# Optimization experiments

Measured on AMD Instinct MI355X. Metric: run time of the kernel, lower is better.

Reference implementation:

```python
import jax, jax.numpy as jnp
import numpy as np

B, N, I = 8, 1024, 64
E, H, D = 2, 2, 128   # edge types, heads per layer, hidden dim
O = 64                # num_outputs
IN1 = E * H * D       # layer-1 filter input dim (concat of layer-0 heads)


def setup_inputs() -> dict:
    key = jax.random.key(0)
    ks = jax.random.split(key, 20)
    s = lambda f: 1.0 / np.sqrt(f)
    inp = {
        "nodes": jax.random.normal(ks[0], (B, N, I), jnp.float32),
        "edges": jax.random.normal(ks[1], (B, N, N, E), jnp.float32) * 0.1,
        "Wemb": jax.random.normal(ks[2], (I, D), jnp.float32) * s(I),
        "bemb": jnp.zeros((D,), jnp.float32),
        # layer 0 params: filter W, att nets a1/a2 (weight + bias), state bias
        "W0":   jax.random.normal(ks[3], (E, H, D, D), jnp.float32) * s(D),
        "A1w0": jax.random.normal(ks[4], (E, H, D), jnp.float32) * s(D),
        "A1b0": jnp.zeros((E, H), jnp.float32),
        "A2w0": jax.random.normal(ks[5], (E, H, D), jnp.float32) * s(D),
        "A2b0": jnp.zeros((E, H), jnp.float32),
        "SB0":  jnp.zeros((E, H, D), jnp.float32),
        # layer 1 params (input dim = E*H*D from concat)
        "W1":   jax.random.normal(ks[6], (E, H, IN1, D), jnp.float32) * s(IN1),
        "A1w1": jax.random.normal(ks[7], (E, H, D), jnp.float32) * s(D),
        "A1b1": jnp.zeros((E, H), jnp.float32),
        "A2w1": jax.random.normal(ks[8], (E, H, D), jnp.float32) * s(D),
        "A2b1": jnp.zeros((E, H), jnp.float32),
        "SB1":  jnp.zeros((E, H, D), jnp.float32),
        "Wout": jax.random.normal(ks[9], (D, O), jnp.float32) * s(D),
        "bout": jnp.zeros((O,), jnp.float32),
    }
    return inp


def _gat_layer(state, edges_ebnn, W, a1w, a1b, a2w, a2b, sb):
    # state: (B,N,Fin); W: (E,H,Fin,D); edges_ebnn: (E,1,B,N,N)
    Wh = jnp.einsum('bni,ehid->ehbnd', state, W)                    # (E,H,B,N,D)
    s1 = jnp.einsum('ehbnd,ehd->ehbn', Wh, a1w) + a1b[:, :, None, None]
    s2 = jnp.einsum('ehbnd,ehd->ehbn', Wh, a2w) + a2b[:, :, None, None]
    att = s1[..., :, None] + s2[..., None, :]                       # a1_i + a2_j
    att = jax.nn.leaky_relu(att, 0.2) + edges_ebnn                  # edge-type bias
    att = jax.nn.softmax(att, axis=-2)                              # torch dim=1 (over i)
    msg = jnp.einsum('ehbij,ehbjd->ehbid', att, Wh)                 # bmm aggregation
    return msg + sb[:, :, None, None, :]                            # (E,H,B,N,D)


def reference(nodes, edges, Wemb, bemb,
              W0, A1w0, A1b0, A2w0, A2b0, SB0,
              W1, A1w1, A1b1, A2w1, A2b1, SB1,
              Wout, bout):
    edges_e = jnp.transpose(edges, (3, 0, 1, 2))[:, None]           # (E,1,B,N,N)
    state = jax.nn.relu(nodes @ Wemb + bemb)                        # SlimFC embedding
    # layer 0: concat heads/edgetypes along feature dim (torch order jj outer, ii inner)
    m0 = _gat_layer(state, edges_e, W0, A1w0, A1b0, A2w0, A2b0, SB0)
    state = jnp.transpose(m0, (2, 3, 0, 1, 4)).reshape(B, N, E * H * D)
    # layer 1 (last): elu then mean over all heads/edgetypes
    m1 = jax.nn.elu(_gat_layer(state, edges_e, W1, A1w1, A1b1, A2w1, A2b1, SB1))
    state = jnp.mean(m1, axis=(0, 1))                               # (B,N,D)
    return state @ Wout + bout                                      # (B,N,O)
```

## Files before the change

### kernel.cpp

```cpp
#include <hip/hip_runtime.h>
#include <hip/hip_bf16.h>
#include <math.h>

#define NB 8
#define NN 1024
#define NI 64
#define EHC 4
#define ND 128
#define NO 64
#define FIN1 512
#define BN 8192

typedef __attribute__((ext_vector_type(8))) short short8;
typedef __attribute__((ext_vector_type(4))) float f32x4;

__device__ __forceinline__ unsigned short f2bf(float f) {
    union { float f; unsigned u; } v; v.f = f;
    unsigned r = v.u + 0x7FFF + ((v.u >> 16) & 1);
    return (unsigned short)(r >> 16);
}

__global__ void prepTk(const float* __restrict__ W0, const float* __restrict__ W1,
                       const float* __restrict__ Wemb, unsigned short* __restrict__ W0T,
                       unsigned short* __restrict__ W1T, unsigned short* __restrict__ WembT) {
    int idx = blockIdx.x * 256 + threadIdx.x;
    if (idx < EHC * ND * ND) {
        int eh = idx >> 14, d = (idx >> 7) & 127, k = idx & 127;
        W0T[idx] = f2bf(W0[((size_t)(eh * ND + k)) * ND + d]);
    }
    int idx1 = idx - EHC * ND * ND;
    if (idx1 >= 0 && idx1 < EHC * ND * FIN1) {
        int eh = idx1 >> 16;
        int r = idx1 & 65535;
        int d = r >> 9, k = r & 511;
        W1T[idx1] = f2bf(W1[((size_t)(eh * FIN1 + k)) * ND + d]);
    }
    int idx2 = idx - (EHC * ND * ND + EHC * ND * FIN1);
    if (idx2 >= 0 && idx2 < ND * NI) {
        int d = idx2 >> 6, k = idx2 & 63;
        WembT[idx2] = f2bf(Wemb[k * ND + d]);
    }
}

__global__ __launch_bounds__(256, 4) void embwh0k(
    const float* __restrict__ nodes, const unsigned short* __restrict__ WembT,
    const float* __restrict__ bemb, const unsigned short* __restrict__ W0T,
    unsigned short* __restrict__ WhT, const float* __restrict__ a1w,
    const float* __restrict__ a1b, const float* __restrict__ a2w,
    const float* __restrict__ a2b, float* __restrict__ s1, float* __restrict__ s2) {
    int id = blockIdx.x;
    int g = id & 7, s_ = id >> 3;
    int eh = s_ & 3;
    int row0 = ((s_ >> 2) * 8 + g) * 32;
    int t = threadIdx.x;
    int w = t >> 6, lane = t & 63;
    int m = lane & 15, quad = lane >> 4;

    __shared__ unsigned short stateL[32 * 136];

    f32x4 accE[2][2];
#pragma unroll
    for (int mt = 0; mt < 2; ++mt)
#pragma unroll
        for (int nt = 0; nt < 2; ++nt) accE[mt][nt] = (f32x4){0.f, 0.f, 0.f, 0.f};
#pragma unroll
    for (int kt = 0; kt < 2; ++kt) {
        short8 aE[2], bE[2];
#pragma unroll
        for (int mt = 0; mt < 2; ++mt) {
            const float* np = nodes + (size_t)(row0 + mt * 16 + m) * NI + kt * 32 + quad * 8;
            f32x4 v0 = *(const f32x4*)np;
            f32x4 v1 = *(const f32x4*)(np + 4);
            union { unsigned short us[8]; short8 s8; } pk;
#pragma unroll
            for (int r = 0; r < 4; ++r) {
                pk.us[r] = f2bf(v0[r]);
                pk.us[r + 4] = f2bf(v1[r]);
            }
            aE[mt] = pk.s8;
        }
#pragma unroll
        for (int nt = 0; nt < 2; ++nt)
            bE[nt] = *(const short8*)(WembT + (w * 32 + nt * 16 + m) * NI + kt * 32 + quad * 8);
#pragma unroll
        for (int mt = 0; mt < 2; ++mt)
#pragma unroll
            for (int nt = 0; nt < 2; ++nt)
                accE[mt][nt] =
                    __builtin_amdgcn_mfma_f32_16x16x32_bf16(aE[mt], bE[nt], accE[mt][nt], 0, 0, 0);
    }
#pragma unroll
    for (int mt = 0; mt < 2; ++mt)
#pragma unroll
        for (int nt = 0; nt < 2; ++nt) {
            int d = w * 32 + nt * 16 + m;
            float bb = bemb[d];
#pragma unroll
            for (int r = 0; r < 4; ++r) {
                float v = fmaxf(accE[mt][nt][r] + bb, 0.f);
                stateL[(mt * 16 + quad * 4 + r) * 136 + d] = f2bf(v);
            }
        }
    __syncthreads();

    f32x4 acc[2][2];
#pragma unroll
    for (int mt = 0; mt < 2; ++mt)
#pragma unroll
        for (int nt = 0; nt < 2; ++nt) acc[mt][nt] = (f32x4){0.f, 0.f, 0.f, 0.f};
#pragma unroll
    for (int k0 = 0; k0 < ND; k0 += 32) {
        short8 a[2], b[2];
#pragma unroll
        for (int mt = 0; mt < 2; ++mt)
            a[mt] = *(const short8*)&stateL[(mt * 16 + m) * 136 + k0 + quad * 8];
#pragma unroll
        for (int nt = 0; nt < 2; ++nt)
            b[nt] = *(const short8*)(W0T + ((size_t)(eh * ND + w * 32 + nt * 16 + m)) * ND +
                                     k0 + quad * 8);
#pragma unroll
        for (int mt = 0; mt < 2; ++mt)
#pragma unroll
            for (int nt = 0; nt < 2; ++nt)
                acc[mt][nt] =
                    __builtin_amdgcn_mfma_f32_16x16x32_bf16(a[mt], b[nt], acc[mt][nt], 0, 0, 0);
    }

    int b_ = row0 >> 10, i0b = row0 & 1023;
    int ehb = eh * NB + b_;
#pragma unroll
    for (int mt = 0; mt < 2; ++mt)
#pragma unroll
        for (int nt = 0; nt < 2; ++nt) {
            int d = w * 32 + nt * 16 + m;
            int i = i0b + mt * 16 + quad * 4;
            union { unsigned short us[4]; unsigned long long u64; } pk;
#pragma unroll
            for (int r = 0; r < 4; ++r) pk.us[r] = f2bf(acc[mt][nt][r]);
            *(unsigned long long*)(WhT + (((size_t)ehb) * ND + d) * NN + i) = pk.u64;
        }
    float w1a = a1w[eh * ND + w * 32 + m], w1b = a1w[eh * ND + w * 32 + 16 + m];
    float w2a = a2w[eh * ND + w * 32 + m], w2b = a2w[eh * ND + w * 32 + 16 + m];
    float p1[2][4], p2[2][4];
#pragma unroll
    for (int mt = 0; mt < 2; ++mt)
#pragma unroll
        for (int r = 0; r < 4; ++r) {
            p1[mt][r] = acc[mt][0][r] * w1a + acc[mt][1][r] * w1b;
            p2[mt][r] = acc[mt][0][r] * w2a + acc[mt][1][r] * w2b;
        }
#pragma unroll
    for (int off = 8; off >= 1; off >>= 1)
#pragma unroll
        for (int mt = 0; mt < 2; ++mt)
#pragma unroll
            for (int r = 0; r < 4; ++r) {
                p1[mt][r] += __shfl_xor(p1[mt][r], off);
                p2[mt][r] += __shfl_xor(p2[mt][r], off);
            }
    __shared__ float sred[2][4][4][8];
    if (m == 0) {
#pragma unroll
        for (int mt = 0; mt < 2; ++mt)
#pragma unroll
            for (int r = 0; r < 4; ++r) {
                sred[0][w][quad][mt * 4 + r] = p1[mt][r];
                sred[1][w][quad][mt * 4 + r] = p2[mt][r];
            }
    }
    __syncthreads();
    if (t < 32) {
        int mt = t >> 4, quad2 = (t >> 2) & 3, r = t & 3;
        int c = mt * 4 + r;
        float v = sred[0][0][quad2][c] + sred[0][1][quad2][c] + sred[0][2][quad2][c] +
                  sred[0][3][quad2][c];
        s1[(size_t)ehb * NN + i0b + t] = v + a1b[eh];
    } else if (t < 64) {
        int tl = t - 32;
        int mt = tl >> 4, quad2 = (tl >> 2) & 3, r = tl & 3;
        int c = mt * 4 + r;
        float v = sred[1][0][quad2][c] + sred[1][1][quad2][c] + sred[1][2][quad2][c] +
                  sred[1][3][quad2][c];
        s2[(size_t)ehb * NN + i0b + tl] = v + a2b[eh];
    }
}

__global__ __launch_bounds__(256, 4) void whgemm1k(
    const unsigned short* __restrict__ state, const unsigned short* __restrict__ WT,
    unsigned short* __restrict__ WhT, const float* __restrict__ a1w,
    const float* __restrict__ a1b, const float* __restrict__ a2w,
    const float* __restrict__ a2b, float* __restrict__ s1, float* __restrict__ s2) {
    int id = blockIdx.x;
    int g = id & 7, s_ = id >> 3;
    int eh = s_ & 3;
    int row0 = ((s_ >> 2) * 8 + g) * 32;
    int t = threadIdx.x;
    int w = t >> 6, lane = t & 63;
    int m = lane & 15, quad = lane >> 4;

    f32x4 acc[2][2];
#pragma unroll
    for (int mt = 0; mt < 2; ++mt)
#pragma unroll
        for (int nt = 0; nt < 2; ++nt) acc[mt][nt] = (f32x4){0.f, 0.f, 0.f, 0.f};

    const unsigned short* Ab = state + (size_t)(row0 + m) * FIN1 + quad * 8;
    const unsigned short* Bb = WT + ((size_t)eh * ND + w * 32 + m) * FIN1 + quad * 8;
#pragma unroll 4
    for (int k0 = 0; k0 < FIN1; k0 += 32) {
        short8 a[2], b[2];
#pragma unroll
        for (int mt = 0; mt < 2; ++mt)
            a[mt] = *(const short8*)(Ab + (size_t)mt * 16 * FIN1 + k0);
#pragma unroll
        for (int nt = 0; nt < 2; ++nt)
            b[nt] = *(const short8*)(Bb + (size_t)nt * 16 * FIN1 + k0);
#pragma unroll
        for (int mt = 0; mt < 2; ++mt)
#pragma unroll
            for (int nt = 0; nt < 2; ++nt)
                acc[mt][nt] =
                    __builtin_amdgcn_mfma_f32_16x16x32_bf16(a[mt], b[nt], acc[mt][nt], 0, 0, 0);
    }
    int b_ = row0 >> 10, i0b = row0 & 1023;
    int ehb = eh * NB + b_;
#pragma unroll
    for (int mt = 0; mt < 2; ++mt)
#pragma unroll
        for (int nt = 0; nt < 2; ++nt) {
            int d = w * 32 + nt * 16 + m;
            int i = i0b + mt * 16 + quad * 4;
            union { unsigned short us[4]; unsigned long long u64; } pk;
#pragma unroll
            for (int r = 0; r < 4; ++r) pk.us[r] = f2bf(acc[mt][nt][r]);
            *(unsigned long long*)(WhT + (((size_t)ehb) * ND + d) * NN + i) = pk.u64;
        }
    float w1a = a1w[eh * ND + w * 32 + m], w1b = a1w[eh * ND + w * 32 + 16 + m];
    float w2a = a2w[eh * ND + w * 32 + m], w2b = a2w[eh * ND + w * 32 + 16 + m];
    float p1[2][4], p2[2][4];
#pragma unroll
    for (int mt = 0; mt < 2; ++mt)
#pragma unroll
        for (int r = 0; r < 4; ++r) {
            p1[mt][r] = acc[mt][0][r] * w1a + acc[mt][1][r] * w1b;
            p2[mt][r] = acc[mt][0][r] * w2a + acc[mt][1][r] * w2b;
        }
#pragma unroll
    for (int off = 8; off >= 1; off >>= 1)
#pragma unroll
        for (int mt = 0; mt < 2; ++mt)
#pragma unroll
            for (int r = 0; r < 4; ++r) {
                p1[mt][r] += __shfl_xor(p1[mt][r], off);
                p2[mt][r] += __shfl_xor(p2[mt][r], off);
            }
    __shared__ float sred[2][4][4][8];
    if (m == 0) {
#pragma unroll
        for (int mt = 0; mt < 2; ++mt)
#pragma unroll
            for (int r = 0; r < 4; ++r) {
                sred[0][w][quad][mt * 4 + r] = p1[mt][r];
                sred[1][w][quad][mt * 4 + r] = p2[mt][r];
            }
    }
    __syncthreads();
    if (t < 32) {
        int mt = t >> 4, quad2 = (t >> 2) & 3, r = t & 3;
        int c = mt * 4 + r;
        float v = sred[0][0][quad2][c] + sred[0][1][quad2][c] + sred[0][2][quad2][c] +
                  sred[0][3][quad2][c];
        s1[(size_t)ehb * NN + i0b + t] = v + a1b[eh];
    } else if (t < 64) {
        int tl = t - 32;
        int mt = tl >> 4, quad2 = (tl >> 2) & 3, r = tl & 3;
        int c = mt * 4 + r;
        float v = sred[1][0][quad2][c] + sred[1][1][quad2][c] + sred[1][2][quad2][c] +
                  sred[1][3][quad2][c];
        s2[(size_t)ehb * NN + i0b + tl] = v + a2b[eh];
    }
}

__global__ __launch_bounds__(256, 4) void colsumk(const float* __restrict__ edges,
                                                  const float* __restrict__ s1,
                                                  const float* __restrict__ s2,
                                                  float* __restrict__ Spart) {
    int jt = blockIdx.x, b = blockIdx.y, ic = blockIdx.z;
    int t = threadIdx.x;
    int jp = t & 31, is = t >> 5;
    int j = jt * 64 + jp * 2;
    __shared__ float s1L[4][128];
    for (int idx = t; idx < 512; idx += 256) {
        int eh = idx >> 7;
        s1L[eh][idx & 127] = s1[((size_t)eh * NB + b) * NN + ic * 128 + (idx & 127)];
    }
    __syncthreads();
    float s2v[4][2], acc4[4][2];
#pragma unroll
    for (int eh = 0; eh < 4; ++eh) {
        s2v[eh][0] = s2[((size_t)eh * NB + b) * NN + j];
        s2v[eh][1] = s2[((size_t)eh * NB + b) * NN + j + 1];
        acc4[eh][0] = 0.f;
        acc4[eh][1] = 0.f;
    }
    const float4* ep = (const float4*)edges +
                       (size_t)(b * NN + ic * 128 + is * 16) * (NN / 2) + jt * 32 + jp;
#pragma unroll 4
    for (int ii = 0; ii < 16; ++ii) {
        float4 ev = ep[(size_t)ii * (NN / 2)];
        float s1v = s1L[0][is * 16 + ii];
#pragma unroll
        for (int eh = 0; eh < 4; ++eh) {
            float sv = s1L[eh][is * 16 + ii];
            float x0 = sv + s2v[eh][0];
            x0 = fmaxf(x0, 0.2f * x0);
            acc4[eh][0] += __expf(x0 + (eh < 2 ? ev.x : ev.y));
            float x1 = sv + s2v[eh][1];
            x1 = fmaxf(x1, 0.2f * x1);
            acc4[eh][1] += __expf(x1 + (eh < 2 ? ev.z : ev.w));
        }
        (void)s1v;
    }
    __shared__ float red[8][4][64];
#pragma unroll
    for (int eh = 0; eh < 4; ++eh) {
        red[is][eh][jp * 2] = acc4[eh][0];
        red[is][eh][jp * 2 + 1] = acc4[eh][1];
    }
    __syncthreads();
    if (t < 256) {
        int eho = t >> 6, jlo = t & 63;
        float Sv = 0.f;
#pragma unroll
        for (int isx = 0; isx < 8; ++isx) Sv += red[isx][eho][jlo];
        Spart[(((size_t)ic * EHC + eho) * NB + b) * NN + jt * 64 + jlo] = Sv;
    }
}

__global__ __launch_bounds__(512, 4) void msgk(const float* __restrict__ edges,
                                               const unsigned short* __restrict__ WhT,
                                               const float* __restrict__ s1,
                                               const float* __restrict__ s2,
                                               const float* __restrict__ Spart,
                                               const float* __restrict__ sb,
                                               unsigned short* __restrict__ out0,
                                               float* __restrict__ out1, int mode) {
    int id = blockIdx.x;
    int b = id & 7;
    int s_ = id >> 3;
    int eh = s_ & 3;
    int itile = s_ >> 2;
    int e = eh >> 1;
    int i0 = itile * 64;
    int t = threadIdx.x;
    int w = t >> 6, lane = t & 63;
    int n = lane & 15, quad = lane >> 4;
    int jl = t & 63, ib = w;

    __shared__ float2 stL[NN];
    __shared__ unsigned short pA[2][64 * 72];

    int base = (eh * NB + b) * NN;
    const size_t pstr = (size_t)EHC * NB * NN;
    for (int jj = t; jj < NN; jj += 512) {
        float S = 0.f;
#pragma unroll
        for (int ic = 0; ic < 8; ++ic) S += Spart[(size_t)ic * pstr + base + jj];
        stL[jj] = make_float2(s2[base + jj], __logf(S));
    }
    float s1r[8];
    {
        const f32x4* sp = (const f32x4*)(s1 + base + i0 + ib * 8);
        f32x4 v0 = sp[0], v1 = sp[1];
#pragma unroll
        for (int r = 0; r < 4; ++r) { s1r[r] = v0[r]; s1r[r + 4] = v1[r]; }
    }

    f32x4 acc[4];
#pragma unroll
    for (int nt = 0; nt < 4; ++nt) acc[nt] = (f32x4){0.f, 0.f, 0.f, 0.f};

    const unsigned short* Ab =
        WhT + ((size_t)base * ND + (size_t)(w * 16 + n) * NN) + quad * 8;
    const float2* ep = (const float2*)edges + (size_t)(b * NN + i0 + ib * 8) * NN + jl;
    __syncthreads();

    float2 evA[8], evB[8];
    short8 aA[2], aB[2];

    auto loadE = [&](float2* ev, int j0) {
#pragma unroll
        for (int q = 0; q < 8; ++q) ev[q] = ep[(size_t)q * NN + j0];
    };
    auto loadA = [&](short8* av, int j0) {
#pragma unroll
        for (int kt = 0; kt < 2; ++kt)
            av[kt] = *(const short8*)(Ab + kt * 32 + j0);
    };
    auto pstep = [&](const float2* ev, const short8* av, int j0, int buf) {
        float2 stj = stL[j0 + jl];
#pragma unroll
        for (int q = 0; q < 8; ++q) {
            float edge = e ? ev[q].y : ev[q].x;
            float x = s1r[q] + stj.x;
            x = fmaxf(x, 0.2f * x);
            pA[buf][(ib * 8 + q) * 72 + jl] = f2bf(__expf(x + edge - stj.y));
        }
        __syncthreads();
#pragma unroll
        for (int kt = 0; kt < 2; ++kt) {
            short8 bv[4];
#pragma unroll
            for (int nt = 0; nt < 4; ++nt)
                bv[nt] = *(const short8*)&pA[buf][(nt * 16 + n) * 72 + kt * 32 + quad * 8];
#pragma unroll
            for (int nt = 0; nt < 4; ++nt)
                acc[nt] =
                    __builtin_amdgcn_mfma_f32_16x16x32_bf16(av[kt], bv[nt], acc[nt], 0, 0, 0);
        }
    };

    loadE(evA, 0);
    loadA(aA, 0);
    for (int sp2 = 0; sp2 < 8; ++sp2) {
        int j0 = sp2 * 128;
        loadE(evB, j0 + 64);
        loadA(aB, j0 + 64);
        pstep(evA, aA, j0, 0);
        if (sp2 < 7) {
            loadE(evA, j0 + 128);
            loadA(aA, j0 + 128);
        }
        pstep(evB, aB, j0 + 64, 1);
    }

    {
        int d0 = w * 16 + quad * 4;
        f32x4 sbv = *(const f32x4*)&sb[eh * ND + d0];
#pragma unroll
        for (int nt = 0; nt < 4; ++nt) {
            int i = i0 + nt * 16 + n;
            if (mode == 0) {
                union { unsigned short us[4]; unsigned long long u64; } pk;
#pragma unroll
                for (int r = 0; r < 4; ++r) pk.us[r] = f2bf(acc[nt][r] + sbv[r]);
                *(unsigned long long*)(out0 + (size_t)(b * NN + i) * FIN1 + eh * ND + d0) =
                    pk.u64;
            } else {
                f32x4 vv;
#pragma unroll
                for (int r = 0; r < 4; ++r) {
                    float v = acc[nt][r] + sbv[r];
                    vv[r] = v > 0.f ? v : expm1f(v);
                }
                *(f32x4*)(out1 + ((size_t)(eh * NB + b) * NN + i) * ND + d0) = vv;
            }
        }
    }
}

__global__ __launch_bounds__(256) void finalk(const float* __restrict__ m1,
                                              const float* __restrict__ Wout,
                                              const float* __restrict__ bout,
                                              float* __restrict__ out) {
    int row0 = blockIdx.x * 16;
    int t = threadIdx.x;
    __shared__ float sF[16 * ND];
    __shared__ float wL[ND * NO];
    const size_t str = (size_t)BN * ND;
    for (int idx = t; idx < 16 * ND; idx += 256) {
        size_t r = (size_t)row0 * ND + idx;
        sF[idx] = 0.25f * (m1[r] + m1[r + str] + m1[r + 2 * str] + m1[r + 3 * str]);
    }
    for (int idx = t; idx < ND * NO; idx += 256) wL[idx] = Wout[idx];
    __syncthreads();
    int o = t & 63;
    int rr = t >> 6;
    float bo = bout[o];
#pragma unroll
    for (int q = 0; q < 4; ++q) {
        int r = rr * 4 + q;
        float acc = 0.f;
#pragma unroll 4
        for (int d = 0; d < ND; ++d) acc += sF[r * ND + d] * wL[d * NO + o];
        out[(size_t)(row0 + r) * NO + o] = acc + bo;
    }
}

extern "C" void kernel_launch(void* const* d_in, const int* in_sizes, int n_in,
                              void* d_out, int out_size, void* d_ws, size_t ws_size,
                              hipStream_t stream) {
    const float* nodes = (const float*)d_in[0];
    const float* edges = (const float*)d_in[1];
    const float* Wemb = (const float*)d_in[2];
    const float* bemb = (const float*)d_in[3];
    const float* W0 = (const float*)d_in[4];
    const float* A1w0 = (const float*)d_in[5];
    const float* A1b0 = (const float*)d_in[6];
    const float* A2w0 = (const float*)d_in[7];
    const float* A2b0 = (const float*)d_in[8];
    const float* SB0 = (const float*)d_in[9];
    const float* W1 = (const float*)d_in[10];
    const float* A1w1 = (const float*)d_in[11];
    const float* A1b1 = (const float*)d_in[12];
    const float* A2w1 = (const float*)d_in[13];
    const float* A2b1 = (const float*)d_in[14];
    const float* SB1 = (const float*)d_in[15];
    const float* Wout = (const float*)d_in[16];
    const float* bout = (const float*)d_in[17];
    float* out = (float*)d_out;

    char* p = (char*)d_ws;
    auto alloc = [&](size_t bytes) {
        char* r = p;
        p += (bytes + 255) & ~(size_t)255;
        return r;
    };
    unsigned short* W0T = (unsigned short*)alloc((size_t)EHC * ND * ND * 2);
    unsigned short* W1T = (unsigned short*)alloc((size_t)EHC * ND * FIN1 * 2);
    unsigned short* WembT = (unsigned short*)alloc((size_t)ND * NI * 2);
    unsigned short* WhT = (unsigned short*)alloc((size_t)EHC * BN * ND * 2);
    unsigned short* state1 = (unsigned short*)alloc((size_t)BN * FIN1 * 2);
    float* s1b = (float*)alloc((size_t)EHC * BN * 4);
    float* s2b = (float*)alloc((size_t)EHC * BN * 4);
    float* Spart = (float*)alloc((size_t)8 * EHC * BN * 4);
    float* m1 = (float*)alloc((size_t)EHC * BN * ND * 4);

    prepTk<<<1312, 256, 0, stream>>>(W0, W1, Wemb, W0T, W1T, WembT);
    embwh0k<<<1024, 256, 0, stream>>>(nodes, WembT, bemb, W0T, WhT, A1w0, A1b0, A2w0, A2b0,
                                      s1b, s2b);
    colsumk<<<dim3(NN / 64, NB, 8), 256, 0, stream>>>(edges, s1b, s2b, Spart);
    msgk<<<512, 512, 0, stream>>>(edges, WhT, s1b, s2b, Spart, SB0, state1, m1, 0);
    whgemm1k<<<1024, 256, 0, stream>>>(state1, W1T, WhT, A1w1, A1b1, A2w1, A2b1, s1b, s2b);
    colsumk<<<dim3(NN / 64, NB, 8), 256, 0, stream>>>(edges, s1b, s2b, Spart);
    msgk<<<512, 512, 0, stream>>>(edges, WhT, s1b, s2b, Spart, SB1, state1, m1, 1);
    finalk<<<BN / 16, 256, 0, stream>>>(m1, Wout, bout, out);
}
```

Before: 275.3 us.

## Convert edges to packed fp16 once and use base-2 exponentials

The first column-sum pass now converts the fp32 edge tensor into a packed fp16 copy, pre-scaled by log2(e), and writes it to a workspace buffer. The later column-sum pass and both message passes read this half-size copy instead of the full fp32 edges. The attention scores s1/s2 are also pre-scaled by log2(e), so exp and log become exp2 and log2. This cuts edge memory traffic in three of the four edge-reading passes, at the cost of an extra write in the first pass and fp16 rounding of the edge bias.

```diff
diff --git a/kernel.cpp b/kernel.cpp
--- a/kernel.cpp
+++ b/kernel.cpp
@@ -1,5 +1,4 @@
 #include <hip/hip_runtime.h>
-#include <hip/hip_bf16.h>
 #include <math.h>
 
 #define NB 8
@@ -10,14 +9,26 @@
 #define NO 64
 #define FIN1 512
 #define BN 8192
+#define LOG2E 1.4426950408889634f
 
 typedef __attribute__((ext_vector_type(8))) short short8;
 typedef __attribute__((ext_vector_type(4))) float f32x4;
+typedef __attribute__((ext_vector_type(2))) unsigned uint32x2;
 
 __device__ __forceinline__ unsigned short f2bf(float f) {
     union { float f; unsigned u; } v; v.f = f;
     unsigned r = v.u + 0x7FFF + ((v.u >> 16) & 1);
     return (unsigned short)(r >> 16);
+}
+__device__ __forceinline__ unsigned short f2h(float f) {
+    union { _Float16 h; unsigned short u; } v;
+    v.h = (_Float16)f;
+    return v.u;
+}
+__device__ __forceinline__ float h2f(unsigned short u) {
+    union { unsigned short u; _Float16 h; } v;
+    v.u = u;
+    return (float)v.h;
 }
 
 __global__ void prepTk(const float* __restrict__ W0, const float* __restrict__ W1,
@@ -174,14 +185,14 @@
         int c = mt * 4 + r;
         float v = sred[0][0][quad2][c] + sred[0][1][quad2][c] + sred[0][2][quad2][c] +
                   sred[0][3][quad2][c];
-        s1[(size_t)ehb * NN + i0b + t] = v + a1b[eh];
+        s1[(size_t)ehb * NN + i0b + t] = (v + a1b[eh]) * LOG2E;
     } else if (t < 64) {
         int tl = t - 32;
         int mt = tl >> 4, quad2 = (tl >> 2) & 3, r = tl & 3;
         int c = mt * 4 + r;
         float v = sred[1][0][quad2][c] + sred[1][1][quad2][c] + sred[1][2][quad2][c] +
                   sred[1][3][quad2][c];
-        s2[(size_t)ehb * NN + i0b + tl] = v + a2b[eh];
+        s2[(size_t)ehb * NN + i0b + tl] = (v + a2b[eh]) * LOG2E;
     }
 }
 
@@ -270,18 +281,20 @@
         int c = mt * 4 + r;
         float v = sred[0][0][quad2][c] + sred[0][1][quad2][c] + sred[0][2][quad2][c] +
                   sred[0][3][quad2][c];
-        s1[(size_t)ehb * NN + i0b + t] = v + a1b[eh];
+        s1[(size_t)ehb * NN + i0b + t] = (v + a1b[eh]) * LOG2E;
     } else if (t < 64) {
         int tl = t - 32;
         int mt = tl >> 4, quad2 = (tl >> 2) & 3, r = tl & 3;
         int c = mt * 4 + r;
         float v = sred[1][0][quad2][c] + sred[1][1][quad2][c] + sred[1][2][quad2][c] +
                   sred[1][3][quad2][c];
-        s2[(size_t)ehb * NN + i0b + tl] = v + a2b[eh];
-    }
-}
-
+        s2[(size_t)ehb * NN + i0b + tl] = (v + a2b[eh]) * LOG2E;
+    }
+}
+
+template <int CONV>
 __global__ __launch_bounds__(256, 4) void colsumk(const float* __restrict__ edges,
+                                                  unsigned* __restrict__ edgesH,
                                                   const float* __restrict__ s1,
                                                   const float* __restrict__ s2,
                                                   float* __restrict__ Spart) {
@@ -303,23 +316,38 @@
         acc4[eh][0] = 0.f;
         acc4[eh][1] = 0.f;
     }
-    const float4* ep = (const float4*)edges +
-                       (size_t)(b * NN + ic * 128 + is * 16) * (NN / 2) + jt * 32 + jp;
+    int irow0 = ic * 128 + is * 16;
+    const float4* ep = (const float4*)edges + (size_t)(b * NN + irow0) * (NN / 2) + jt * 32 + jp;
+    unsigned* ehw = edgesH + (size_t)(b * NN + irow0) * NN + j;
 #pragma unroll 4
     for (int ii = 0; ii < 16; ++ii) {
-        float4 ev = ep[(size_t)ii * (NN / 2)];
-        float s1v = s1L[0][is * 16 + ii];
+        float e00, e10, e01, e11;
+        if (CONV) {
+            float4 ev = ep[(size_t)ii * (NN / 2)];
+            unsigned p0 = (unsigned)f2h(ev.x * LOG2E) | ((unsigned)f2h(ev.y * LOG2E) << 16);
+            unsigned p1 = (unsigned)f2h(ev.z * LOG2E) | ((unsigned)f2h(ev.w * LOG2E) << 16);
+            *(uint32x2*)(ehw + (size_t)ii * NN) = (uint32x2){p0, p1};
+            e00 = h2f((unsigned short)(p0 & 0xffff));
+            e10 = h2f((unsigned short)(p0 >> 16));
+            e01 = h2f((unsigned short)(p1 & 0xffff));
+            e11 = h2f((unsigned short)(p1 >> 16));
+        } else {
+            uint32x2 pk = *(const uint32x2*)(ehw + (size_t)ii * NN);
+            e00 = h2f((unsigned short)(pk.x & 0xffff));
+            e10 = h2f((unsigned short)(pk.x >> 16));
+            e01 = h2f((unsigned short)(pk.y & 0xffff));
+            e11 = h2f((unsigned short)(pk.y >> 16));
+        }
 #pragma unroll
         for (int eh = 0; eh < 4; ++eh) {
             float sv = s1L[eh][is * 16 + ii];
             float x0 = sv + s2v[eh][0];
             x0 = fmaxf(x0, 0.2f * x0);
-            acc4[eh][0] += __expf(x0 + (eh < 2 ? ev.x : ev.y));
+            acc4[eh][0] += __builtin_exp2f(x0 + (eh < 2 ? e00 : e10));
             float x1 = sv + s2v[eh][1];
             x1 = fmaxf(x1, 0.2f * x1);
-            acc4[eh][1] += __expf(x1 + (eh < 2 ? ev.z : ev.w));
-        }
-        (void)s1v;
+            acc4[eh][1] += __builtin_exp2f(x1 + (eh < 2 ? e01 : e11));
+        }
     }
     __shared__ float red[8][4][64];
 #pragma unroll
@@ -337,7 +365,7 @@
     }
 }
 
-__global__ __launch_bounds__(512, 4) void msgk(const float* __restrict__ edges,
+__global__ __launch_bounds__(512, 4) void msgk(const unsigned* __restrict__ edgesH,
                                                const unsigned short* __restrict__ WhT,
                                                const float* __restrict__ s1,
                                                const float* __restrict__ s2,
@@ -366,7 +394,7 @@
         float S = 0.f;
 #pragma unroll
         for (int ic = 0; ic < 8; ++ic) S += Spart[(size_t)ic * pstr + base + jj];
-        stL[jj] = make_float2(s2[base + jj], __logf(S));
+        stL[jj] = make_float2(s2[base + jj], __builtin_log2f(S));
     }
     float s1r[8];
     {
@@ -382,13 +410,13 @@
 
     const unsigned short* Ab =
         WhT + ((size_t)base * ND + (size_t)(w * 16 + n) * NN) + quad * 8;
-    const float2* ep = (const float2*)edges + (size_t)(b * NN + i0 + ib * 8) * NN + jl;
-    __syncthreads();
-
-    float2 evA[8], evB[8];
+    const unsigned* ep = edgesH + (size_t)(b * NN + i0 + ib * 8) * NN + jl;
+    __syncthreads();
+
+    unsigned evA[8], evB[8];
     short8 aA[2], aB[2];
 
-    auto loadE = [&](float2* ev, int j0) {
+    auto loadE = [&](unsigned* ev, int j0) {
 #pragma unroll
         for (int q = 0; q < 8; ++q) ev[q] = ep[(size_t)q * NN + j0];
     };
@@ -397,14 +425,14 @@
         for (int kt = 0; kt < 2; ++kt)
             av[kt] = *(const short8*)(Ab + kt * 32 + j0);
     };
-    auto pstep = [&](const float2* ev, const short8* av, int j0, int buf) {
+    auto pstep = [&](const unsigned* ev, const short8* av, int j0, int buf) {
         float2 stj = stL[j0 + jl];
 #pragma unroll
         for (int q = 0; q < 8; ++q) {
-            float edge = e ? ev[q].y : ev[q].x;
+            float edge = h2f((unsigned short)(e ? (ev[q] >> 16) : (ev[q] & 0xffff)));
             float x = s1r[q] + stj.x;
             x = fmaxf(x, 0.2f * x);
-            pA[buf][(ib * 8 + q) * 72 + jl] = f2bf(__expf(x + edge - stj.y));
+            pA[buf][(ib * 8 + q) * 72 + jl] = f2bf(__builtin_exp2f(x + edge - stj.y));
         }
         __syncthreads();
 #pragma unroll
@@ -525,14 +553,15 @@
     float* s2b = (float*)alloc((size_t)EHC * BN * 4);
     float* Spart = (float*)alloc((size_t)8 * EHC * BN * 4);
     float* m1 = (float*)alloc((size_t)EHC * BN * ND * 4);
+    unsigned* edgesH = (unsigned*)alloc((size_t)NB * NN * NN * 4);
 
     prepTk<<<1312, 256, 0, stream>>>(W0, W1, Wemb, W0T, W1T, WembT);
     embwh0k<<<1024, 256, 0, stream>>>(nodes, WembT, bemb, W0T, WhT, A1w0, A1b0, A2w0, A2b0,
                                       s1b, s2b);
-    colsumk<<<dim3(NN / 64, NB, 8), 256, 0, stream>>>(edges, s1b, s2b, Spart);
-    msgk<<<512, 512, 0, stream>>>(edges, WhT, s1b, s2b, Spart, SB0, state1, m1, 0);
+    colsumk<1><<<dim3(NN / 64, NB, 8), 256, 0, stream>>>(edges, edgesH, s1b, s2b, Spart);
+    msgk<<<512, 512, 0, stream>>>(edgesH, WhT, s1b, s2b, Spart, SB0, state1, m1, 0);
     whgemm1k<<<1024, 256, 0, stream>>>(state1, W1T, WhT, A1w1, A1b1, A2w1, A2b1, s1b, s2b);
-    colsumk<<<dim3(NN / 64, NB, 8), 256, 0, stream>>>(edges, s1b, s2b, Spart);
-    msgk<<<512, 512, 0, stream>>>(edges, WhT, s1b, s2b, Spart, SB1, state1, m1, 1);
+    colsumk<0><<<dim3(NN / 64, NB, 8), 256, 0, stream>>>(edges, edgesH, s1b, s2b, Spart);
+    msgk<<<512, 512, 0, stream>>>(edgesH, WhT, s1b, s2b, Spart, SB1, state1, m1, 1);
     finalk<<<BN / 16, 256, 0, stream>>>(m1, Wout, bout, out);
 }
```

Measured after the change: 267.4 us. 1.03x faster.
